# Optimization experiments

Hardware: AMD Instinct MI355X
Metric: run time of the kernel (lower is better)

The kernel has to match this reference:

```python
import jax, jax.numpy as jnp
import numpy as np

B, T = 4, 8192
C = 64            # dilation_channels (also embedding size)
S = 256           # skip_dims
V = 256           # waveform_categories (8-bit mu-law)
CENTER = 128      # waveform_center_cat
DILATIONS = [1, 2, 4, 8, 16, 32, 64, 128, 256, 512] * 3  # 3 blocks, 30 layers
L = len(DILATIONS)


def setup_inputs() -> dict:
    key = jax.random.key(0)
    ks = jax.random.split(key, 16)
    waveform = jax.random.randint(ks[0], (B, T, 1), 0, V, dtype=jnp.int32)
    waveform_lens = jax.random.randint(ks[1], (B,), 0, T, dtype=jnp.int32)
    s = 0.05
    embed = jax.random.normal(ks[2], (V, C), dtype=jnp.float32) * s
    # conv_w[l, 0] applies to x[t-d], conv_w[l, 1] to x[t] (kernel_size=2)
    conv_w = jax.random.normal(ks[3], (L, 2, C, 2 * C), dtype=jnp.float32) * s
    conv_b = jnp.zeros((L, 2 * C), dtype=jnp.float32)
    res_w = jax.random.normal(ks[4], (L, C, C), dtype=jnp.float32) * s
    res_b = jnp.zeros((L, C), dtype=jnp.float32)
    skip_w = jax.random.normal(ks[5], (L, C, S), dtype=jnp.float32) * s
    skip_b = jnp.zeros((L, S), dtype=jnp.float32)
    w0 = jax.random.normal(ks[6], (S, V), dtype=jnp.float32) * s
    b0 = jnp.zeros((V,), dtype=jnp.float32)
    w1 = jax.random.normal(ks[7], (V, V), dtype=jnp.float32) * s
    b1 = jnp.zeros((V,), dtype=jnp.float32)
    return dict(waveform=waveform, waveform_lens=waveform_lens, embed=embed,
                conv_w=conv_w, conv_b=conv_b, res_w=res_w, res_b=res_b,
                skip_w=skip_w, skip_b=skip_b, w0=w0, b0=b0, w1=w1, b1=b1)


def _wavenet(wf, lens, embed, conv_w, conv_b, res_w, res_b, skip_w, skip_b, w0, b0, w1, b1):
    labels = wf[..., 0]                                          # (B, T) int
    # shift right with <go> = center category
    inp = jnp.concatenate(
        [jnp.full((B, 1), CENTER, dtype=labels.dtype), labels[:, :-1]], axis=1)
    x = embed[inp]                                               # (B, T, C)
    skip_sum = jnp.zeros((B, T, S), dtype=x.dtype)
    for i, d in enumerate(DILATIONS):
        # dilated causal conv, kernel 2: y[t] = x[t-d] @ W0 + x[t] @ W1 + b
        x_shift = jnp.pad(x, ((0, 0), (d, 0), (0, 0)))[:, :T]    # left pad d
        h = (jnp.einsum('btc,cf->btf', x_shift, conv_w[i, 0])
             + jnp.einsum('btc,cf->btf', x, conv_w[i, 1]) + conv_b[i])
        gate = jnp.tanh(h[..., :C]) * jax.nn.sigmoid(h[..., C:])  # (B, T, C)
        x = x + jnp.einsum('btc,cd->btd', gate, res_w[i]) + res_b[i]
        skip_sum = skip_sum + jnp.einsum('btc,cs->bts', gate, skip_w[i]) + skip_b[i]
    hid0 = jax.nn.relu(jnp.einsum('bts,sv->btv', skip_sum, w0) + b0)
    logits = jnp.einsum('btv,vu->btu', hid0, w1) + b1            # (B, T, V)
    logp = jax.nn.log_softmax(logits, axis=-1)
    ce = -jnp.take_along_axis(logp, labels[..., None], axis=-1)[..., 0]  # (B, T)
    mask = (jnp.arange(T)[None, :] < lens[:, None]).astype(logits.dtype)
    loss = jnp.sum(ce * mask) / jnp.maximum(jnp.sum(mask), 1.0)
    return loss


def reference(waveform, waveform_lens, embed, conv_w, conv_b, res_w, res_b,
              skip_w, skip_b, w0, b0, w1, b1):
    return _wavenet(waveform, waveform_lens, embed, conv_w, conv_b, res_w,
                    res_b, skip_w, skip_b, w0, b0, w1, b1)
```

## Files before the change

### kernel.cpp

```cpp
#include <hip/hip_runtime.h>

#define NB 4
#define NT 8192
#define NC 64
#define NS 256
#define NV 256
#define NL 30

typedef __attribute__((ext_vector_type(8))) short bf16x8;
typedef __attribute__((ext_vector_type(4))) float f32x4;
typedef unsigned short ushort_t;

#define MFMA(a, b, c) __builtin_amdgcn_mfma_f32_16x16x32_bf16(a, b, c, 0, 0, 0)

#define OFF_WCAT 0
#define SZ_WCAT  (NL * 16384)
#define OFF_RW   (OFF_WCAT + SZ_WCAT)
#define SZ_RW    (NL * 4096)
#define OFF_SWG  (OFF_RW + SZ_RW)
#define SZ_SWG   (6 * 81920)
#define OFF_W0   (OFF_SWG + SZ_SWG)
#define OFF_W1   (OFF_W0 + 65536)
#define TOTAL_W  (OFF_W1 + 65536)
#define N_PREP   (TOTAL_W + 1792)

#define X_ELEMS  (NB * NT * NC)
#define SK_ELEMS (NB * NT * NS)
#define G_ELEMS  (NB * NT * NC)

#define WS_SMALL ((size_t)(2 * X_ELEMS + SK_ELEMS + 5 * G_ELEMS + TOTAL_W) * 2 \
                  + 1792 * 4)
#define WS_BIG   ((size_t)(2 * X_ELEMS + 30 * G_ELEMS + TOTAL_W) * 2 + 1792 * 4)

__device__ inline ushort_t f2bu(float f) {
  union { float f; unsigned u; } v; v.f = f;
  unsigned r = v.u + 0x7FFFu + ((v.u >> 16) & 1u);
  return (ushort_t)(r >> 16);
}
__device__ inline float b2f(ushort_t h) {
  union { unsigned u; float f; } v; v.u = ((unsigned)h) << 16; return v.f;
}

__global__ void sentinel_kernel(float* __restrict__ out) {
  if (threadIdx.x == 0) out[0] = -1234.0f;
}

__global__ __launch_bounds__(256) void prep_kernel(
    const float* __restrict__ cw, const float* __restrict__ rw,
    const float* __restrict__ sw, const float* __restrict__ w0,
    const float* __restrict__ w1, const float* __restrict__ sb_all,
    ushort_t* __restrict__ wt, float* __restrict__ sbg,
    float* __restrict__ out0)
{
  int idx = blockIdx.x * 256 + threadIdx.x;
  if (idx == 0) out0[0] = 0.f;
  if (idx >= N_PREP) return;
  if (idx >= TOTAL_W) {
    int j = idx - TOTAL_W;
    if (j < 1536) {
      int g = j >> 8, n = j & 255;
      float s = 0.f;
#pragma unroll
      for (int jj = 0; jj < 5; ++jj) s += sb_all[(5 * g + jj) * 256 + n];
      sbg[j] = s;
    } else {
      int n = j - 1536;
      float s = 0.f;
      for (int jj = 0; jj < NL; ++jj) s += sb_all[jj * 256 + n];
      sbg[j] = s;
    }
    return;
  }
  float v;
  if (idx < OFF_RW) {
    int e = idx; int l = e >> 14; int r = e & 16383;
    int kk = r >> 12, n = (r >> 5) & 127, j = r & 31;
    int k = kk * 32 + j, tap = k >> 6, c = k & 63;
    v = cw[(((l * 2 + tap) << 6) + c) * 128 + n];
  } else if (idx < OFF_SWG) {
    int e = idx - OFF_RW; int l = e >> 12; int r = e & 4095;
    int kk = r >> 11, n = (r >> 5) & 63, j = r & 31;
    int k = kk * 32 + j;
    v = rw[((l << 6) + k) * 64 + n];
  } else if (idx < OFF_W0) {
    int e = idx - OFF_SWG; int g = e / 81920; int r = e % 81920;
    int kk = r >> 13; int rem = r & 8191;
    int n = rem >> 5, jj = rem & 31;
    int k = kk * 32 + jj;
    v = sw[(size_t)(320 * g + k) * 256 + n];
  } else if (idx < OFF_W1) {
    int e = idx - OFF_W0;
    int kk = e >> 13; int rem = e & 8191;
    int n = rem >> 5, jj = rem & 31;
    int k = kk * 32 + jj;
    v = w0[k * 256 + n];
  } else {
    int e = idx - OFF_W1;
    int kk = e >> 13; int rem = e & 8191;
    int n = rem >> 5, jj = rem & 31;
    int k = kk * 32 + jj;
    v = w1[k * 256 + n];
  }
  wt[idx] = f2bu(v);
}

__global__ __launch_bounds__(256) void embed_kernel(
    const int* __restrict__ wf, const float* __restrict__ embed,
    ushort_t* __restrict__ x0)
{
  const int bidx = blockIdx.x;
  const int bb = bidx >> 7;
  const int t0 = (bidx & 127) << 6;
  const int pos0 = bb * NT + t0;
  for (int e = threadIdx.x; e < 64 * 64; e += 256) {
    int p = e >> 6, c = e & 63;
    int t = t0 + p;
    int id = (t == 0) ? 128 : wf[bb * NT + t - 1];
    x0[(size_t)(pos0 + p) * NC + c] = f2bu(embed[id * NC + c]);
  }
}

__global__ __launch_bounds__(384) void chain5_kernel(
    const ushort_t* __restrict__ xin, ushort_t* __restrict__ xout,
    ushort_t* __restrict__ gates,
    const ushort_t* __restrict__ wt,
    const float* __restrict__ cb_all, const float* __restrict__ rb_all,
    int l0, const int* __restrict__ wf, const float* __restrict__ embf)
{
  __shared__ __align__(16) ushort_t xt[96][72];
  __shared__ __align__(16) ushort_t gt[96][72];

  const int tid = threadIdx.x;
  const int w = tid >> 6, lane = tid & 63;
  const int quad = lane >> 4, c16 = lane & 15;
  const int bb = blockIdx.x >> 7;
  const int t0 = (blockIdx.x & 127) << 6;
  const size_t row0 = (size_t)bb * NT;

#pragma unroll
  for (int i = 0; i < 2; ++i) {
    int e = tid + i * 384;
    int r = e >> 3, c0 = (e & 7) * 8;
    int t = t0 - 32 + r;
    bf16x8 v;
    if (t >= 0) {
      if (embf) {
        int id = (t == 0) ? 128 : wf[row0 + t - 1];
        const float* ep = embf + id * NC + c0;
#pragma unroll
        for (int jj = 0; jj < 8; ++jj) v[jj] = (short)f2bu(ep[jj]);
      } else {
        v = *(const bf16x8*)(xin + (row0 + t) * 64 + c0);
      }
    } else { bf16x8 z = {0, 0, 0, 0, 0, 0, 0, 0}; v = z; }
    *(bf16x8*)&xt[r][c0] = v;
  }
  __syncthreads();

  for (int j = 0; j < 5; ++j) {
    const int l = l0 + j;
    const int d = 1 << j;
    const ushort_t* wcat = wt + OFF_WCAT + l * 16384;
    const ushort_t* rww  = wt + OFF_RW + l * 4096;
    const float* cb = cb_all + l * 128;
    const float* rb = rb_all + l * 64;

    bf16x8 af[4];
    {
      int lr = w * 16 + c16;
#pragma unroll
      for (int kk = 0; kk < 4; ++kk) {
        int rr = (kk < 2) ? lr - d : lr;
        int ch = (kk & 1) * 32 + quad * 8;
        if (rr >= 0) af[kk] = *(const bf16x8*)&xt[rr][ch];
        else { bf16x8 z = {0, 0, 0, 0, 0, 0, 0, 0}; af[kk] = z; }
      }
    }
    __syncthreads();

    {
      f32x4 acc[8];
#pragma unroll
      for (int q = 0; q < 4; ++q) {
        float ba = cb[q * 16 + c16], bs = cb[q * 16 + c16 + 64];
        f32x4 va = {ba, ba, ba, ba}, vb = {bs, bs, bs, bs};
        acc[q] = va; acc[4 + q] = vb;
      }
#pragma unroll
      for (int kk = 0; kk < 4; ++kk) {
        const ushort_t* wp = wcat + kk * 4096 + c16 * 32 + quad * 8;
#pragma unroll
        for (int q = 0; q < 4; ++q) {
          acc[q]     = MFMA(af[kk], *(const bf16x8*)(wp + q * 512), acc[q]);
          acc[4 + q] = MFMA(af[kk], *(const bf16x8*)(wp + q * 512 + 2048), acc[4 + q]);
        }
      }
#pragma unroll
      for (int q = 0; q < 4; ++q)
#pragma unroll
        for (int r = 0; r < 4; ++r) {
          float e2 = __expf(2.f * acc[q][r]);
          float th = (e2 - 1.f) / (e2 + 1.f);
          float sg = 1.f / (1.f + __expf(-acc[4 + q][r]));
          gt[w * 16 + quad * 4 + r][q * 16 + c16] = f2bu(th * sg);
        }

      bf16x8 gf0 = *(const bf16x8*)&gt[w * 16 + c16][quad * 8];
      bf16x8 gf1 = *(const bf16x8*)&gt[w * 16 + c16][32 + quad * 8];

      f32x4 acc2[4];
#pragma unroll
      for (int q = 0; q < 4; ++q) {
        float bv = rb[q * 16 + c16];
        f32x4 z = {bv, bv, bv, bv};
        acc2[q] = z;
      }
      const ushort_t* wp2 = rww + c16 * 32 + quad * 8;
#pragma unroll
      for (int q = 0; q < 4; ++q)
        acc2[q] = MFMA(gf0, *(const bf16x8*)(wp2 + q * 512), acc2[q]);
#pragma unroll
      for (int q = 0; q < 4; ++q)
        acc2[q] = MFMA(gf1, *(const bf16x8*)(wp2 + q * 512 + 2048), acc2[q]);
#pragma unroll
      for (int q = 0; q < 4; ++q) {
        int n = q * 16 + c16;
#pragma unroll
        for (int r = 0; r < 4; ++r) {
          int rowi = w * 16 + quad * 4 + r;
          xt[rowi][n] = f2bu(b2f(xt[rowi][n]) + acc2[q][r]);
        }
      }
    }
    __syncthreads();

    {
      ushort_t* gslot = gates + (size_t)j * G_ELEMS;
      int e = tid;
      {
        int r = e >> 3, c0 = (e & 7) * 8;
        *(bf16x8*)(gslot + (row0 + t0 + r) * 64 + c0) =
            *(const bf16x8*)&gt[32 + r][c0];
      }
      e = tid + 384;
      if (e < 512) {
        int r = e >> 3, c0 = (e & 7) * 8;
        *(bf16x8*)(gslot + (row0 + t0 + r) * 64 + c0) =
            *(const bf16x8*)&gt[32 + r][c0];
      }
    }
  }
  __syncthreads();

  {
    int e = tid;
    {
      int r = e >> 3, c0 = (e & 7) * 8;
      *(bf16x8*)(xout + (row0 + t0 + r) * 64 + c0) = *(const bf16x8*)&xt[32 + r][c0];
    }
    e = tid + 384;
    if (e < 512) {
      int r = e >> 3, c0 = (e & 7) * 8;
      *(bf16x8*)(xout + (row0 + t0 + r) * 64 + c0) = *(const bf16x8*)&xt[32 + r][c0];
    }
  }
}

__global__ __launch_bounds__(256, 4) void layer_kernel(
    const ushort_t* __restrict__ xin, ushort_t* __restrict__ xout,
    ushort_t* __restrict__ gate_out,
    const ushort_t* __restrict__ wcat_s, const float* __restrict__ cb,
    const ushort_t* __restrict__ rww,    const float* __restrict__ rb,
    int d, int write_res)
{
  __shared__ __align__(16) ushort_t lwc[16384];
  __shared__ __align__(16) ushort_t gt[64][72];

  const int tid = threadIdx.x;
  const int w = tid >> 6, lane = tid & 63;
  const int quad = lane >> 4, c16 = lane & 15;
  const int bb = blockIdx.x >> 7;
  const int t0 = (blockIdx.x & 127) << 6;
  const int tb = t0 + w * 16;
  const size_t row0 = (size_t)bb * NT;

  {
    bf16x8* dst = (bf16x8*)lwc;
    const bf16x8* s1 = (const bf16x8*)wcat_s;
#pragma unroll
    for (int i = 0; i < 8; ++i) dst[tid + i * 256] = s1[tid + i * 256];
  }

  const int tA = tb + c16;
  bf16x8 af[4];
#pragma unroll
  for (int kk = 0; kk < 4; ++kk) {
    int ts = (kk < 2) ? (tA - d) : tA;
    int ch = (kk & 1) * 32 + quad * 8;
    if (ts >= 0) {
      af[kk] = *(const bf16x8*)(xin + (row0 + ts) * 64 + ch);
    } else {
      bf16x8 z = {0, 0, 0, 0, 0, 0, 0, 0};
      af[kk] = z;
    }
  }
  __syncthreads();

#pragma unroll
  for (int q = 0; q < 4; ++q) {
    int na = q * 16 + c16;
    int nb2 = na + 64;
    float ba = cb[na], bs = cb[nb2];
    f32x4 va = {ba, ba, ba, ba}, vb = {bs, bs, bs, bs};
#pragma unroll
    for (int kk = 0; kk < 4; ++kk) {
      va = MFMA(af[kk], *(const bf16x8*)&lwc[kk * 4096 + na * 32 + quad * 8], va);
      vb = MFMA(af[kk], *(const bf16x8*)&lwc[kk * 4096 + nb2 * 32 + quad * 8], vb);
    }
#pragma unroll
    for (int r = 0; r < 4; ++r) {
      float e2 = __expf(2.f * va[r]);
      float th = (e2 - 1.f) / (e2 + 1.f);
      float sg = 1.f / (1.f + __expf(-vb[r]));
      gt[w * 16 + quad * 4 + r][q * 16 + c16] = f2bu(th * sg);
    }
  }

  bf16x8 gf0 = *(const bf16x8*)&gt[w * 16 + c16][quad * 8];
  bf16x8 gf1 = *(const bf16x8*)&gt[w * 16 + c16][32 + quad * 8];

  if (write_res) {
    const ushort_t* wp2 = rww + c16 * 32 + quad * 8;
#pragma unroll
    for (int q = 0; q < 4; ++q) {
      int n = q * 16 + c16;
      float bv = rb[n];
      f32x4 acc = {bv, bv, bv, bv};
      acc = MFMA(gf0, *(const bf16x8*)(wp2 + q * 512), acc);
      acc = MFMA(gf1, *(const bf16x8*)(wp2 + q * 512 + 2048), acc);
#pragma unroll
      for (int r = 0; r < 4; ++r) {
        size_t idx = (row0 + tb + quad * 4 + r) * 64 + n;
        xout[idx] = f2bu(b2f(xin[idx]) + acc[r]);
      }
    }
  }

#pragma unroll
  for (int i = 0; i < 2; ++i) {
    int e = lane + i * 64;
    int rr = w * 16 + (e >> 3), c0 = (e & 7) * 8;
    *(bf16x8*)(gate_out + (row0 + t0 + rr) * 64 + c0) = *(const bf16x8*)&gt[rr][c0];
  }
}

__global__ __launch_bounds__(384) void chain5hi_kernel(
    const ushort_t* __restrict__ xin, ushort_t* __restrict__ xout,
    ushort_t* __restrict__ gates,
    const ushort_t* __restrict__ wt,
    const float* __restrict__ cb_all, const float* __restrict__ rb_all,
    int lbase, int write_x)
{
  __shared__ __align__(16) ushort_t xt[96][72];
  __shared__ __align__(16) ushort_t gt[96][72];

  const int tid = threadIdx.x;
  const int w = tid >> 6, lane = tid & 63;
  const int quad = lane >> 4, c16 = lane & 15;
  const int bb = blockIdx.x >> 7;
  const int sub = blockIdx.x & 127;
  const int k = sub & 31;
  const int i0 = (sub >> 5) << 6;
  const size_t row0 = (size_t)bb * NT;

#pragma unroll
  for (int i = 0; i < 2; ++i) {
    int e = tid + i * 384;
    int r = e >> 3, c0 = (e & 7) * 8;
    int ii = i0 + r - 32;
    bf16x8 v;
    if (ii >= 0) v = *(const bf16x8*)(xin + (row0 + (size_t)ii * 32 + k) * 64 + c0);
    else { bf16x8 z = {0, 0, 0, 0, 0, 0, 0, 0}; v = z; }
    *(bf16x8*)&xt[r][c0] = v;
  }
  __syncthreads();

  for (int j = 0; j < 5; ++j) {
    const int l = lbase + j;
    const int d = 1 << j;
    const ushort_t* wcat = wt + OFF_WCAT + l * 16384;
    const ushort_t* rww  = wt + OFF_RW + l * 4096;
    const float* cb = cb_all + l * 128;
    const float* rb = rb_all + l * 64;

    bf16x8 af[4];
    {
      int lr = w * 16 + c16;
#pragma unroll
      for (int kk = 0; kk < 4; ++kk) {
        int rr = (kk < 2) ? lr - d : lr;
        int ch = (kk & 1) * 32 + quad * 8;
        if (rr >= 0) af[kk] = *(const bf16x8*)&xt[rr][ch];
        else { bf16x8 z = {0, 0, 0, 0, 0, 0, 0, 0}; af[kk] = z; }
      }
    }
    __syncthreads();

    {
      f32x4 acc[8];
#pragma unroll
      for (int q = 0; q < 4; ++q) {
        float ba = cb[q * 16 + c16], bs = cb[q * 16 + c16 + 64];
        f32x4 va = {ba, ba, ba, ba}, vb = {bs, bs, bs, bs};
        acc[q] = va; acc[4 + q] = vb;
      }
#pragma unroll
      for (int kk = 0; kk < 4; ++kk) {
        const ushort_t* wp = wcat + kk * 4096 + c16 * 32 + quad * 8;
#pragma unroll
        for (int q = 0; q < 4; ++q) {
          acc[q]     = MFMA(af[kk], *(const bf16x8*)(wp + q * 512), acc[q]);
          acc[4 + q] = MFMA(af[kk], *(const bf16x8*)(wp + q * 512 + 2048), acc[4 + q]);
        }
      }
#pragma unroll
      for (int q = 0; q < 4; ++q)
#pragma unroll
        for (int r = 0; r < 4; ++r) {
          float e2 = __expf(2.f * acc[q][r]);
          float th = (e2 - 1.f) / (e2 + 1.f);
          float sg = 1.f / (1.f + __expf(-acc[4 + q][r]));
          gt[w * 16 + quad * 4 + r][q * 16 + c16] = f2bu(th * sg);
        }

      if (write_x || j < 4) {
        bf16x8 gf0 = *(const bf16x8*)&gt[w * 16 + c16][quad * 8];
        bf16x8 gf1 = *(const bf16x8*)&gt[w * 16 + c16][32 + quad * 8];

        f32x4 acc2[4];
#pragma unroll
        for (int q = 0; q < 4; ++q) {
          float bv = rb[q * 16 + c16];
          f32x4 z = {bv, bv, bv, bv};
          acc2[q] = z;
        }
        const ushort_t* wp2 = rww + c16 * 32 + quad * 8;
#pragma unroll
        for (int q = 0; q < 4; ++q)
          acc2[q] = MFMA(gf0, *(const bf16x8*)(wp2 + q * 512), acc2[q]);
#pragma unroll
        for (int q = 0; q < 4; ++q)
          acc2[q] = MFMA(gf1, *(const bf16x8*)(wp2 + q * 512 + 2048), acc2[q]);
#pragma unroll
        for (int q = 0; q < 4; ++q) {
          int n = q * 16 + c16;
#pragma unroll
          for (int r = 0; r < 4; ++r) {
            int rowi = w * 16 + quad * 4 + r;
            xt[rowi][n] = f2bu(b2f(xt[rowi][n]) + acc2[q][r]);
          }
        }
      }
    }
    __syncthreads();

    {
      ushort_t* gslot = gates + (size_t)j * G_ELEMS;
      int e = tid;
      {
        int r = e >> 3, c0 = (e & 7) * 8;
        *(bf16x8*)(gslot + (row0 + (size_t)(i0 + r) * 32 + k) * 64 + c0) =
            *(const bf16x8*)&gt[32 + r][c0];
      }
      e = tid + 384;
      if (e < 512) {
        int r = e >> 3, c0 = (e & 7) * 8;
        *(bf16x8*)(gslot + (row0 + (size_t)(i0 + r) * 32 + k) * 64 + c0) =
            *(const bf16x8*)&gt[32 + r][c0];
      }
    }
  }
  __syncthreads();

  if (write_x) {
    int e = tid;
    {
      int r = e >> 3, c0 = (e & 7) * 8;
      *(bf16x8*)(xout + (row0 + (size_t)(i0 + r) * 32 + k) * 64 + c0) =
          *(const bf16x8*)&xt[32 + r][c0];
    }
    e = tid + 384;
    if (e < 512) {
      int r = e >> 3, c0 = (e & 7) * 8;
      *(bf16x8*)(xout + (row0 + (size_t)(i0 + r) * 32 + k) * 64 + c0) =
          *(const bf16x8*)&xt[32 + r][c0];
    }
  }
}

__global__ __launch_bounds__(256) void skip30_head_kernel(
    const ushort_t* __restrict__ gates,
    const ushort_t* __restrict__ wt,
    const float* __restrict__ sbtot,
    const float* __restrict__ b0, const float* __restrict__ b1,
    const int* __restrict__ wf, const int* __restrict__ lens,
    float* __restrict__ loss)
{
  __shared__ __align__(16) ushort_t wbuf[2][8192];
  __shared__ __align__(16) ushort_t tile[64][264];
  const int tid = threadIdx.x;
  const int w = tid >> 6, lane = tid & 63;
  const int quad = lane >> 4, c16 = lane & 15;
  const int bb = blockIdx.x >> 7;
  const int t0 = (blockIdx.x & 127) << 6;
  const int tb = t0 + w * 16;
  const size_t row0 = (size_t)bb * NT;
  const int mylen = lens[bb];
  const ushort_t* swg = wt + OFF_SWG;

  f32x4 acc[16];
#pragma unroll
  for (int nt = 0; nt < 16; ++nt) { f32x4 z = {0.f, 0.f, 0.f, 0.f}; acc[nt] = z; }

  const size_t arow = (row0 + tb + c16) * 64;
  bf16x8 wreg[4];
#pragma unroll
  for (int i = 0; i < 4; ++i)
    wreg[i] = ((const bf16x8*)swg)[tid + i * 256];
  bf16x8 af = *(const bf16x8*)(gates + arow + quad * 8);
  int cur = 0;

  for (int kk = 0; kk < 60; ++kk) {
#pragma unroll
    for (int i = 0; i < 4; ++i)
      ((bf16x8*)wbuf[cur])[tid + i * 256] = wreg[i];
    int kn = (kk + 1 < 60) ? kk + 1 : 59;
#pragma unroll
    for (int i = 0; i < 4; ++i)
      wreg[i] = ((const bf16x8*)(swg + (size_t)kn * 8192))[tid + i * 256];
    bf16x8 afn = *(const bf16x8*)(gates + (size_t)(kn >> 1) * G_ELEMS + arow +
                                  (kn & 1) * 32 + quad * 8);
    __syncthreads();
    const ushort_t* wp = wbuf[cur] + c16 * 32 + quad * 8;
#pragma unroll
    for (int nt = 0; nt < 16; ++nt)
      acc[nt] = MFMA(af, *(const bf16x8*)(wp + nt * 512), acc[nt]);
    af = afn; cur ^= 1;
  }

#pragma unroll
  for (int nt = 0; nt < 16; ++nt) {
    int n = nt * 16 + c16;
    float sbn = sbtot[n];
#pragma unroll
    for (int r = 0; r < 4; ++r)
      tile[w * 16 + quad * 4 + r][n] = f2bu(acc[nt][r] + sbn);
  }

  const ushort_t* w0T = wt + OFF_W0;
  f32x4 accA[16];
#pragma unroll
  for (int nt = 0; nt < 16; ++nt) {
    float bv = b0[nt * 16 + c16];
    f32x4 z = {bv, bv, bv, bv};
    accA[nt] = z;
  }
  for (int kk = 0; kk < 8; ++kk) {
#pragma unroll
    for (int i = 0; i < 4; ++i)
      ((bf16x8*)wbuf[0])[tid + i * 256] = ((const bf16x8*)(w0T + kk * 8192))[tid + i * 256];
    __syncthreads();
    bf16x8 hf = *(const bf16x8*)&tile[w * 16 + c16][kk * 32 + quad * 8];
    const ushort_t* wp = wbuf[0] + c16 * 32 + quad * 8;
#pragma unroll
    for (int nt = 0; nt < 16; ++nt)
      accA[nt] = MFMA(hf, *(const bf16x8*)(wp + nt * 512), accA[nt]);
    __syncthreads();
  }
#pragma unroll
  for (int nt = 0; nt < 16; ++nt)
#pragma unroll
    for (int r = 0; r < 4; ++r)
      tile[w * 16 + quad * 4 + r][nt * 16 + c16] = f2bu(fmaxf(accA[nt][r], 0.f));

  const ushort_t* w1T = wt + OFF_W1;
  f32x4 acc2[16];
#pragma unroll
  for (int nt = 0; nt < 16; ++nt) {
    float bv = b1[nt * 16 + c16];
    f32x4 z = {bv, bv, bv, bv};
    acc2[nt] = z;
  }
  for (int kk = 0; kk < 8; ++kk) {
#pragma unroll
    for (int i = 0; i < 4; ++i)
      ((bf16x8*)wbuf[0])[tid + i * 256] = ((const bf16x8*)(w1T + kk * 8192))[tid + i * 256];
    __syncthreads();
    bf16x8 hf = *(const bf16x8*)&tile[w * 16 + c16][kk * 32 + quad * 8];
    const ushort_t* wp = wbuf[0] + c16 * 32 + quad * 8;
#pragma unroll
    for (int nt = 0; nt < 16; ++nt)
      acc2[nt] = MFMA(hf, *(const bf16x8*)(wp + nt * 512), acc2[nt]);
    __syncthreads();
  }

  int lblv[4];
#pragma unroll
  for (int r = 0; r < 4; ++r)
    lblv[r] = wf[row0 + tb + quad * 4 + r];

  float local = 0.f;
#pragma unroll
  for (int r = 0; r < 4; ++r) {
    float m = -1e30f, tv = -1e30f;
#pragma unroll
    for (int nt = 0; nt < 16; ++nt) {
      float v = acc2[nt][r];
      m = fmaxf(m, v);
      if (lblv[r] == nt * 16 + c16) tv = v;
    }
#pragma unroll
    for (int dd = 1; dd < 16; dd <<= 1) m = fmaxf(m, __shfl_xor(m, dd));
    float s = 0.f;
#pragma unroll
    for (int nt = 0; nt < 16; ++nt) s += __expf(acc2[nt][r] - m);
#pragma unroll
    for (int dd = 1; dd < 16; dd <<= 1) {
      s += __shfl_xor(s, dd);
      tv = fmaxf(tv, __shfl_xor(tv, dd));
    }
    int t = tb + quad * 4 + r;
    if (c16 == 0 && t < mylen) local += (m + __logf(s)) - tv;
  }
#pragma unroll
  for (int dd = 1; dd < 64; dd <<= 1) local += __shfl_xor(local, dd);
  if (lane == 0 && local != 0.f) atomicAdd(loss, local);
}

__global__ __launch_bounds__(256) void skip_kernel(
    ushort_t* __restrict__ skip, const ushort_t* __restrict__ gates,
    const ushort_t* __restrict__ swg, const float* __restrict__ sbg,
    int first)
{
  __shared__ __align__(16) ushort_t wbuf[8192];
  const int tid = threadIdx.x;
  const int w = tid >> 6, lane = tid & 63;
  const int quad = lane >> 4, c16 = lane & 15;
  const int bb = blockIdx.x >> 7;
  const int t0 = (blockIdx.x & 127) << 6;
  const int tb = t0 + w * 16;
  const size_t row0 = (size_t)bb * NT;

  f32x4 acc[16];
#pragma unroll
  for (int nt = 0; nt < 16; ++nt) { f32x4 z = {0.f, 0.f, 0.f, 0.f}; acc[nt] = z; }

  const size_t arow = (row0 + tb + c16) * 64;
  for (int kk = 0; kk < 10; ++kk) {
#pragma unroll
    for (int i = 0; i < 4; ++i)
      ((bf16x8*)wbuf)[tid + i * 256] = ((const bf16x8*)(swg + kk * 8192))[tid + i * 256];
    __syncthreads();

    int slot = kk >> 1;
    bf16x8 af = *(const bf16x8*)(gates + (size_t)slot * G_ELEMS + arow +
                                 (kk & 1) * 32 + quad * 8);
    const ushort_t* wp = wbuf + c16 * 32 + quad * 8;
#pragma unroll
    for (int nt = 0; nt < 16; ++nt)
      acc[nt] = MFMA(af, *(const bf16x8*)(wp + nt * 512), acc[nt]);
    __syncthreads();
  }

#pragma unroll
  for (int nt = 0; nt < 16; ++nt) {
    int n = nt * 16 + c16;
    float sbn = sbg[n];
#pragma unroll
    for (int r = 0; r < 4; ++r) {
      size_t idx = (row0 + tb + quad * 4 + r) * 256 + n;
      float old = first ? 0.f : b2f(skip[idx]);
      skip[idx] = f2bu(old + acc[nt][r] + sbn);
    }
  }
}

__global__ __launch_bounds__(256) void head_kernel(
    const ushort_t* __restrict__ skip,
    const ushort_t* __restrict__ w0T, const float* __restrict__ b0,
    const ushort_t* __restrict__ w1T, const float* __restrict__ b1,
    const int* __restrict__ wf, const int* __restrict__ lens,
    float* __restrict__ loss)
{
  __shared__ __align__(16) ushort_t wbuf[8192];
  __shared__ __align__(16) ushort_t tile[64][264];
  const int tid = threadIdx.x;
  const int w = tid >> 6, lane = tid & 63;
  const int quad = lane >> 4, c16 = lane & 15;
  const int bb = blockIdx.x >> 7;
  const int t0 = (blockIdx.x & 127) << 6;
  const int tb = t0 + w * 16;
  const size_t row0 = (size_t)bb * NT;
  const int mylen = lens[bb];

#pragma unroll
  for (int i = 0; i < 8; ++i) {
    int e = lane + i * 64;
    int r = e >> 5, c0 = (e & 31) * 8;
    *(bf16x8*)&tile[w * 16 + r][c0] =
        *(const bf16x8*)(skip + (row0 + t0 + w * 16 + r) * 256 + c0);
  }

  f32x4 accA[16];
#pragma unroll
  for (int nt = 0; nt < 16; ++nt) {
    float bv = b0[nt * 16 + c16];
    f32x4 z = {bv, bv, bv, bv};
    accA[nt] = z;
  }
  for (int kk = 0; kk < 8; ++kk) {
#pragma unroll
    for (int i = 0; i < 4; ++i)
      ((bf16x8*)wbuf)[tid + i * 256] = ((const bf16x8*)(w0T + kk * 8192))[tid + i * 256];
    __syncthreads();
    bf16x8 af = *(const bf16x8*)&tile[w * 16 + c16][kk * 32 + quad * 8];
    const ushort_t* wp = wbuf + c16 * 32 + quad * 8;
#pragma unroll
    for (int nt = 0; nt < 16; ++nt)
      accA[nt] = MFMA(af, *(const bf16x8*)(wp + nt * 512), accA[nt]);
    __syncthreads();
  }
#pragma unroll
  for (int nt = 0; nt < 16; ++nt)
#pragma unroll
    for (int r = 0; r < 4; ++r)
      tile[w * 16 + quad * 4 + r][nt * 16 + c16] = f2bu(fmaxf(accA[nt][r], 0.f));

  f32x4 acc2[16];
#pragma unroll
  for (int nt = 0; nt < 16; ++nt) {
    float bv = b1[nt * 16 + c16];
    f32x4 z = {bv, bv, bv, bv};
    acc2[nt] = z;
  }
  for (int kk = 0; kk < 8; ++kk) {
#pragma unroll
    for (int i = 0; i < 4; ++i)
      ((bf16x8*)wbuf)[tid + i * 256] = ((const bf16x8*)(w1T + kk * 8192))[tid + i * 256];
    __syncthreads();
    bf16x8 hf = *(const bf16x8*)&tile[w * 16 + c16][kk * 32 + quad * 8];
    const ushort_t* wp = wbuf + c16 * 32 + quad * 8;
#pragma unroll
    for (int nt = 0; nt < 16; ++nt)
      acc2[nt] = MFMA(hf, *(const bf16x8*)(wp + nt * 512), acc2[nt]);
    __syncthreads();
  }

  int lblv[4];
#pragma unroll
  for (int r = 0; r < 4; ++r)
    lblv[r] = wf[row0 + tb + quad * 4 + r];

  float local = 0.f;
#pragma unroll
  for (int r = 0; r < 4; ++r) {
    float m = -1e30f, tv = -1e30f;
#pragma unroll
    for (int nt = 0; nt < 16; ++nt) {
      float v = acc2[nt][r];
      m = fmaxf(m, v);
      if (lblv[r] == nt * 16 + c16) tv = v;
    }
#pragma unroll
    for (int dd = 1; dd < 16; dd <<= 1) m = fmaxf(m, __shfl_xor(m, dd));
    float s = 0.f;
#pragma unroll
    for (int nt = 0; nt < 16; ++nt) s += __expf(acc2[nt][r] - m);
#pragma unroll
    for (int dd = 1; dd < 16; dd <<= 1) {
      s += __shfl_xor(s, dd);
      tv = fmaxf(tv, __shfl_xor(tv, dd));
    }
    int t = tb + quad * 4 + r;
    if (c16 == 0 && t < mylen) local += (m + __logf(s)) - tv;
  }
#pragma unroll
  for (int dd = 1; dd < 64; dd <<= 1) local += __shfl_xor(local, dd);
  if (lane == 0 && local != 0.f) atomicAdd(loss, local);
}

__global__ void finalize_kernel(const int* __restrict__ lens,
                                float* __restrict__ out)
{
  if (threadIdx.x == 0) {
    float den = 0.f;
    for (int b = 0; b < NB; ++b) {
      int l = lens[b];
      if (l > NT) l = NT;
      den += (float)l;
    }
    out[0] = out[0] / fmaxf(den, 1.f);
  }
}

extern "C" void kernel_launch(void* const* d_in, const int* in_sizes, int n_in,
                              void* d_out, int out_size, void* d_ws, size_t ws_size,
                              hipStream_t stream) {
  const int*   wf     = (const int*)d_in[0];
  const int*   lens   = (const int*)d_in[1];
  const float* embed  = (const float*)d_in[2];
  const float* conv_w = (const float*)d_in[3];
  const float* conv_b = (const float*)d_in[4];
  const float* res_w  = (const float*)d_in[5];
  const float* res_b  = (const float*)d_in[6];
  const float* skip_w = (const float*)d_in[7];
  const float* skip_b = (const float*)d_in[8];
  const float* w0     = (const float*)d_in[9];
  const float* b0     = (const float*)d_in[10];
  const float* w1     = (const float*)d_in[11];
  const float* b1     = (const float*)d_in[12];

  float* out = (float*)d_out;
  if (ws_size < WS_SMALL) {
    sentinel_kernel<<<1, 64, 0, stream>>>(out);
    return;
  }
  const bool big = (ws_size >= WS_BIG);

  static const int dil[NL] = {1, 2, 4, 8, 16, 32, 64, 128, 256, 512,
                              1, 2, 4, 8, 16, 32, 64, 128, 256, 512,
                              1, 2, 4, 8, 16, 32, 64, 128, 256, 512};

  if (big) {
    ushort_t* x0    = (ushort_t*)d_ws;
    ushort_t* x1    = x0 + X_ELEMS;
    ushort_t* gates = x1 + X_ELEMS;
    ushort_t* wt    = gates + 30 * (size_t)G_ELEMS;
    float*    sbg   = (float*)(wt + TOTAL_W);

    prep_kernel<<<(N_PREP + 255) / 256, 256, 0, stream>>>(
        conv_w, res_w, skip_w, w0, w1, skip_b, wt, sbg, out);

    const ushort_t* xin = x0;
    ushort_t* xout = x1;
    for (int blk = 0; blk < 3; ++blk) {
      const int l0 = blk * 10;
      chain5_kernel<<<512, 384, 0, stream>>>(
          xin, xout, gates + (size_t)l0 * G_ELEMS,
          wt, conv_b, res_b, l0, wf, blk == 0 ? embed : nullptr);
      { const ushort_t* t = xout; xout = (ushort_t*)xin; xin = t; }
      for (int l = l0 + 5; l < l0 + 10; ++l) {
        layer_kernel<<<512, 256, 0, stream>>>(
            xin, xout, gates + (size_t)l * G_ELEMS,
            wt + OFF_WCAT + l * 16384, conv_b + l * 128,
            wt + OFF_RW + l * 4096,    res_b + l * 64,
            dil[l], l < NL - 1 ? 1 : 0);
        { const ushort_t* t = xout; xout = (ushort_t*)xin; xin = t; }
      }
    }

    skip30_head_kernel<<<512, 256, 0, stream>>>(
        gates, wt, sbg + 1536, b0, b1, wf, lens, out);
    finalize_kernel<<<1, 64, 0, stream>>>(lens, out);
  } else {
    ushort_t* x0    = (ushort_t*)d_ws;
    ushort_t* x1    = x0 + X_ELEMS;
    ushort_t* skip  = x1 + X_ELEMS;
    ushort_t* gates = skip + SK_ELEMS;
    ushort_t* wt    = gates + 5 * (size_t)G_ELEMS;
    float*    sbg   = (float*)(wt + TOTAL_W);

    prep_kernel<<<(N_PREP + 255) / 256, 256, 0, stream>>>(
        conv_w, res_w, skip_w, w0, w1, skip_b, wt, sbg, out);
    embed_kernel<<<512, 256, 0, stream>>>(wf, embed, x0);

    const ushort_t* xin = x0;
    ushort_t* xout = x1;
    for (int blk = 0; blk < 3; ++blk) {
      const int l0 = blk * 10;
      chain5_kernel<<<512, 384, 0, stream>>>(
          xin, xout, gates, wt, conv_b, res_b, l0, wf, nullptr);
      { const ushort_t* t = xout; xout = (ushort_t*)xin; xin = t; }
      skip_kernel<<<512, 256, 0, stream>>>(
          skip, gates, wt + OFF_SWG + (size_t)(2 * blk) * 81920,
          sbg + (size_t)(2 * blk) * 256, blk == 0 ? 1 : 0);
      chain5hi_kernel<<<512, 384, 0, stream>>>(
          xin, xout, gates, wt, conv_b, res_b, l0 + 5, blk < 2 ? 1 : 0);
      { const ushort_t* t = xout; xout = (ushort_t*)xin; xin = t; }
      skip_kernel<<<512, 256, 0, stream>>>(
          skip, gates, wt + OFF_SWG + (size_t)(2 * blk + 1) * 81920,
          sbg + (size_t)(2 * blk + 1) * 256, 0);
    }

    head_kernel<<<512, 256, 0, stream>>>(
        skip, wt + OFF_W0, b0, wt + OFF_W1, b1, wf, lens, out);
    finalize_kernel<<<1, 64, 0, stream>>>(lens, out);
  }
}
```

Measured before the change: 416.3 us.

## Fuse high-dilation layers into strided chain kernels keeping residual in LDS

Replaces the five per-layer launches for dilations 32..512 with two fused kernels (2 and 3 layers) that gather a strided time subsequence (stride 32 or 128) so each dilation becomes a small local shift within an LDS tile. The residual stream stays in shared memory across the fused layers and is written out once, which cuts launches and global round trips of x. It adds halo recomputation (80 rows loaded for 64 outputs), strided global access patterns, and reads weights directly from global instead of staging them in LDS.

Result: slower. 435.2 us (+4.5%).

```diff
diff --git a/kernel.cpp b/kernel.cpp
--- a/kernel.cpp
+++ b/kernel.cpp
@@ -266,91 +266,273 @@
   }
 }
 
-__global__ __launch_bounds__(256, 4) void layer_kernel(
+__global__ __launch_bounds__(320) void chain2hi_kernel(
     const ushort_t* __restrict__ xin, ushort_t* __restrict__ xout,
-    ushort_t* __restrict__ gate_out,
-    const ushort_t* __restrict__ wcat_s, const float* __restrict__ cb,
-    const ushort_t* __restrict__ rww,    const float* __restrict__ rb,
-    int d, int write_res)
+    ushort_t* __restrict__ gates,
+    const ushort_t* __restrict__ wt,
+    const float* __restrict__ cb_all, const float* __restrict__ rb_all,
+    int lbase)
 {
-  __shared__ __align__(16) ushort_t lwc[16384];
-  __shared__ __align__(16) ushort_t gt[64][72];
+  __shared__ __align__(16) ushort_t xt[80][72];
+  __shared__ __align__(16) ushort_t gt[80][72];
 
   const int tid = threadIdx.x;
   const int w = tid >> 6, lane = tid & 63;
   const int quad = lane >> 4, c16 = lane & 15;
   const int bb = blockIdx.x >> 7;
-  const int t0 = (blockIdx.x & 127) << 6;
-  const int tb = t0 + w * 16;
+  const int sub = blockIdx.x & 127;
+  const int k = sub & 31;
+  const int i0 = (sub >> 5) << 6;
   const size_t row0 = (size_t)bb * NT;
 
-  {
-    bf16x8* dst = (bf16x8*)lwc;
-    const bf16x8* s1 = (const bf16x8*)wcat_s;
-#pragma unroll
-    for (int i = 0; i < 8; ++i) dst[tid + i * 256] = s1[tid + i * 256];
-  }
-
-  const int tA = tb + c16;
-  bf16x8 af[4];
-#pragma unroll
-  for (int kk = 0; kk < 4; ++kk) {
-    int ts = (kk < 2) ? (tA - d) : tA;
-    int ch = (kk & 1) * 32 + quad * 8;
-    if (ts >= 0) {
-      af[kk] = *(const bf16x8*)(xin + (row0 + ts) * 64 + ch);
-    } else {
-      bf16x8 z = {0, 0, 0, 0, 0, 0, 0, 0};
-      af[kk] = z;
-    }
+#pragma unroll
+  for (int i = 0; i < 2; ++i) {
+    int e = tid + i * 320;
+    int r = e >> 3, c0 = (e & 7) * 8;
+    int ii = i0 + r - 16;
+    bf16x8 v;
+    if (ii >= 0) v = *(const bf16x8*)(xin + (row0 + (size_t)ii * 32 + k) * 64 + c0);
+    else { bf16x8 z = {0, 0, 0, 0, 0, 0, 0, 0}; v = z; }
+    *(bf16x8*)&xt[r][c0] = v;
   }
   __syncthreads();
 
-#pragma unroll
-  for (int q = 0; q < 4; ++q) {
-    int na = q * 16 + c16;
-    int nb2 = na + 64;
-    float ba = cb[na], bs = cb[nb2];
-    f32x4 va = {ba, ba, ba, ba}, vb = {bs, bs, bs, bs};
-#pragma unroll
-    for (int kk = 0; kk < 4; ++kk) {
-      va = MFMA(af[kk], *(const bf16x8*)&lwc[kk * 4096 + na * 32 + quad * 8], va);
-      vb = MFMA(af[kk], *(const bf16x8*)&lwc[kk * 4096 + nb2 * 32 + quad * 8], vb);
-    }
-#pragma unroll
-    for (int r = 0; r < 4; ++r) {
-      float e2 = __expf(2.f * va[r]);
-      float th = (e2 - 1.f) / (e2 + 1.f);
-      float sg = 1.f / (1.f + __expf(-vb[r]));
-      gt[w * 16 + quad * 4 + r][q * 16 + c16] = f2bu(th * sg);
-    }
-  }
-
-  bf16x8 gf0 = *(const bf16x8*)&gt[w * 16 + c16][quad * 8];
-  bf16x8 gf1 = *(const bf16x8*)&gt[w * 16 + c16][32 + quad * 8];
-
-  if (write_res) {
-    const ushort_t* wp2 = rww + c16 * 32 + quad * 8;
-#pragma unroll
-    for (int q = 0; q < 4; ++q) {
-      int n = q * 16 + c16;
-      float bv = rb[n];
-      f32x4 acc = {bv, bv, bv, bv};
-      acc = MFMA(gf0, *(const bf16x8*)(wp2 + q * 512), acc);
-      acc = MFMA(gf1, *(const bf16x8*)(wp2 + q * 512 + 2048), acc);
-#pragma unroll
-      for (int r = 0; r < 4; ++r) {
-        size_t idx = (row0 + tb + quad * 4 + r) * 64 + n;
-        xout[idx] = f2bu(b2f(xin[idx]) + acc[r]);
-      }
-    }
-  }
+  for (int j = 0; j < 2; ++j) {
+    const int l = lbase + j;
+    const int d = 1 << j;
+    const ushort_t* wcat = wt + OFF_WCAT + l * 16384;
+    const ushort_t* rww  = wt + OFF_RW + l * 4096;
+    const float* cb = cb_all + l * 128;
+    const float* rb = rb_all + l * 64;
+
+    bf16x8 af[4];
+    {
+      int lr = w * 16 + c16;
+#pragma unroll
+      for (int kk = 0; kk < 4; ++kk) {
+        int rr = (kk < 2) ? lr - d : lr;
+        int ch = (kk & 1) * 32 + quad * 8;
+        if (rr >= 0) af[kk] = *(const bf16x8*)&xt[rr][ch];
+        else { bf16x8 z = {0, 0, 0, 0, 0, 0, 0, 0}; af[kk] = z; }
+      }
+    }
+    __syncthreads();
+
+    {
+      f32x4 acc[8];
+#pragma unroll
+      for (int q = 0; q < 4; ++q) {
+        float ba = cb[q * 16 + c16], bs = cb[q * 16 + c16 + 64];
+        f32x4 va = {ba, ba, ba, ba}, vb = {bs, bs, bs, bs};
+        acc[q] = va; acc[4 + q] = vb;
+      }
+#pragma unroll
+      for (int kk = 0; kk < 4; ++kk) {
+        const ushort_t* wp = wcat + kk * 4096 + c16 * 32 + quad * 8;
+#pragma unroll
+        for (int q = 0; q < 4; ++q) {
+          acc[q]     = MFMA(af[kk], *(const bf16x8*)(wp + q * 512), acc[q]);
+          acc[4 + q] = MFMA(af[kk], *(const bf16x8*)(wp + q * 512 + 2048), acc[4 + q]);
+        }
+      }
+#pragma unroll
+      for (int q = 0; q < 4; ++q)
+#pragma unroll
+        for (int r = 0; r < 4; ++r) {
+          float e2 = __expf(2.f * acc[q][r]);
+          float th = (e2 - 1.f) / (e2 + 1.f);
+          float sg = 1.f / (1.f + __expf(-acc[4 + q][r]));
+          gt[w * 16 + quad * 4 + r][q * 16 + c16] = f2bu(th * sg);
+        }
+
+      bf16x8 gf0 = *(const bf16x8*)&gt[w * 16 + c16][quad * 8];
+      bf16x8 gf1 = *(const bf16x8*)&gt[w * 16 + c16][32 + quad * 8];
+
+      f32x4 acc2[4];
+#pragma unroll
+      for (int q = 0; q < 4; ++q) {
+        float bv = rb[q * 16 + c16];
+        f32x4 z = {bv, bv, bv, bv};
+        acc2[q] = z;
+      }
+      const ushort_t* wp2 = rww + c16 * 32 + quad * 8;
+#pragma unroll
+      for (int q = 0; q < 4; ++q)
+        acc2[q] = MFMA(gf0, *(const bf16x8*)(wp2 + q * 512), acc2[q]);
+#pragma unroll
+      for (int q = 0; q < 4; ++q)
+        acc2[q] = MFMA(gf1, *(const bf16x8*)(wp2 + q * 512 + 2048), acc2[q]);
+#pragma unroll
+      for (int q = 0; q < 4; ++q) {
+        int n = q * 16 + c16;
+#pragma unroll
+        for (int r = 0; r < 4; ++r) {
+          int rowi = w * 16 + quad * 4 + r;
+          xt[rowi][n] = f2bu(b2f(xt[rowi][n]) + acc2[q][r]);
+        }
+      }
+    }
+    __syncthreads();
+
+    {
+      ushort_t* gslot = gates + (size_t)l * G_ELEMS;
+#pragma unroll
+      for (int i = 0; i < 2; ++i) {
+        int e = tid + i * 320;
+        if (e < 512) {
+          int r = e >> 3, c0 = (e & 7) * 8;
+          *(bf16x8*)(gslot + (row0 + (size_t)(i0 + r) * 32 + k) * 64 + c0) =
+              *(const bf16x8*)&gt[16 + r][c0];
+        }
+      }
+    }
+  }
+  __syncthreads();
 
 #pragma unroll
   for (int i = 0; i < 2; ++i) {
-    int e = lane + i * 64;
-    int rr = w * 16 + (e >> 3), c0 = (e & 7) * 8;
-    *(bf16x8*)(gate_out + (row0 + t0 + rr) * 64 + c0) = *(const bf16x8*)&gt[rr][c0];
+    int e = tid + i * 320;
+    if (e < 512) {
+      int r = e >> 3, c0 = (e & 7) * 8;
+      *(bf16x8*)(xout + (row0 + (size_t)(i0 + r) * 32 + k) * 64 + c0) =
+          *(const bf16x8*)&xt[16 + r][c0];
+    }
+  }
+}
+
+__global__ __launch_bounds__(320) void chain3hi_kernel(
+    const ushort_t* __restrict__ xin, ushort_t* __restrict__ xout,
+    ushort_t* __restrict__ gates,
+    const ushort_t* __restrict__ wt,
+    const float* __restrict__ cb_all, const float* __restrict__ rb_all,
+    int lbase, int write_x)
+{
+  __shared__ __align__(16) ushort_t xt[80][72];
+  __shared__ __align__(16) ushort_t gt[80][72];
+
+  const int tid = threadIdx.x;
+  const int w = tid >> 6, lane = tid & 63;
+  const int quad = lane >> 4, c16 = lane & 15;
+  const int bb = blockIdx.x >> 7;
+  const int k2 = blockIdx.x & 127;
+  const size_t row0 = (size_t)bb * NT;
+
+#pragma unroll
+  for (int i = 0; i < 2; ++i) {
+    int e = tid + i * 320;
+    int r = e >> 3, c0 = (e & 7) * 8;
+    int ii = r - 16;
+    bf16x8 v;
+    if (ii >= 0) v = *(const bf16x8*)(xin + (row0 + (size_t)ii * 128 + k2) * 64 + c0);
+    else { bf16x8 z = {0, 0, 0, 0, 0, 0, 0, 0}; v = z; }
+    *(bf16x8*)&xt[r][c0] = v;
+  }
+  __syncthreads();
+
+  for (int j = 0; j < 3; ++j) {
+    const int l = lbase + j;
+    const int d = 1 << j;
+    const ushort_t* wcat = wt + OFF_WCAT + l * 16384;
+    const ushort_t* rww  = wt + OFF_RW + l * 4096;
+    const float* cb = cb_all + l * 128;
+    const float* rb = rb_all + l * 64;
+
+    bf16x8 af[4];
+    {
+      int lr = w * 16 + c16;
+#pragma unroll
+      for (int kk = 0; kk < 4; ++kk) {
+        int rr = (kk < 2) ? lr - d : lr;
+        int ch = (kk & 1) * 32 + quad * 8;
+        if (rr >= 0) af[kk] = *(const bf16x8*)&xt[rr][ch];
+        else { bf16x8 z = {0, 0, 0, 0, 0, 0, 0, 0}; af[kk] = z; }
+      }
+    }
+    __syncthreads();
+
+    {
+      f32x4 acc[8];
+#pragma unroll
+      for (int q = 0; q < 4; ++q) {
+        float ba = cb[q * 16 + c16], bs = cb[q * 16 + c16 + 64];
+        f32x4 va = {ba, ba, ba, ba}, vb = {bs, bs, bs, bs};
+        acc[q] = va; acc[4 + q] = vb;
+      }
+#pragma unroll
+      for (int kk = 0; kk < 4; ++kk) {
+        const ushort_t* wp = wcat + kk * 4096 + c16 * 32 + quad * 8;
+#pragma unroll
+        for (int q = 0; q < 4; ++q) {
+          acc[q]     = MFMA(af[kk], *(const bf16x8*)(wp + q * 512), acc[q]);
+          acc[4 + q] = MFMA(af[kk], *(const bf16x8*)(wp + q * 512 + 2048), acc[4 + q]);
+        }
+      }
+#pragma unroll
+      for (int q = 0; q < 4; ++q)
+#pragma unroll
+        for (int r = 0; r < 4; ++r) {
+          float e2 = __expf(2.f * acc[q][r]);
+          float th = (e2 - 1.f) / (e2 + 1.f);
+          float sg = 1.f / (1.f + __expf(-acc[4 + q][r]));
+          gt[w * 16 + quad * 4 + r][q * 16 + c16] = f2bu(th * sg);
+        }
+
+      if (write_x || j < 2) {
+        bf16x8 gf0 = *(const bf16x8*)&gt[w * 16 + c16][quad * 8];
+        bf16x8 gf1 = *(const bf16x8*)&gt[w * 16 + c16][32 + quad * 8];
+
+        f32x4 acc2[4];
+#pragma unroll
+        for (int q = 0; q < 4; ++q) {
+          float bv = rb[q * 16 + c16];
+          f32x4 z = {bv, bv, bv, bv};
+          acc2[q] = z;
+        }
+        const ushort_t* wp2 = rww + c16 * 32 + quad * 8;
+#pragma unroll
+        for (int q = 0; q < 4; ++q)
+          acc2[q] = MFMA(gf0, *(const bf16x8*)(wp2 + q * 512), acc2[q]);
+#pragma unroll
+        for (int q = 0; q < 4; ++q)
+          acc2[q] = MFMA(gf1, *(const bf16x8*)(wp2 + q * 512 + 2048), acc2[q]);
+#pragma unroll
+        for (int q = 0; q < 4; ++q) {
+          int n = q * 16 + c16;
+#pragma unroll
+          for (int r = 0; r < 4; ++r) {
+            int rowi = w * 16 + quad * 4 + r;
+            xt[rowi][n] = f2bu(b2f(xt[rowi][n]) + acc2[q][r]);
+          }
+        }
+      }
+    }
+    __syncthreads();
+
+    {
+      ushort_t* gslot = gates + (size_t)l * G_ELEMS;
+#pragma unroll
+      for (int i = 0; i < 2; ++i) {
+        int e = tid + i * 320;
+        if (e < 512) {
+          int r = e >> 3, c0 = (e & 7) * 8;
+          *(bf16x8*)(gslot + (row0 + (size_t)r * 128 + k2) * 64 + c0) =
+              *(const bf16x8*)&gt[16 + r][c0];
+        }
+      }
+    }
+  }
+  __syncthreads();
+
+  if (write_x) {
+#pragma unroll
+    for (int i = 0; i < 2; ++i) {
+      int e = tid + i * 320;
+      if (e < 512) {
+        int r = e >> 3, c0 = (e & 7) * 8;
+        *(bf16x8*)(xout + (row0 + (size_t)r * 128 + k2) * 64 + c0) =
+            *(const bf16x8*)&xt[16 + r][c0];
+      }
+    }
   }
 }
 
@@ -827,10 +1009,6 @@
   }
   const bool big = (ws_size >= WS_BIG);
 
-  static const int dil[NL] = {1, 2, 4, 8, 16, 32, 64, 128, 256, 512,
-                              1, 2, 4, 8, 16, 32, 64, 128, 256, 512,
-                              1, 2, 4, 8, 16, 32, 64, 128, 256, 512};
-
   if (big) {
     ushort_t* x0    = (ushort_t*)d_ws;
     ushort_t* x1    = x0 + X_ELEMS;
@@ -849,14 +1027,12 @@
           xin, xout, gates + (size_t)l0 * G_ELEMS,
           wt, conv_b, res_b, l0, wf, blk == 0 ? embed : nullptr);
       { const ushort_t* t = xout; xout = (ushort_t*)xin; xin = t; }
-      for (int l = l0 + 5; l < l0 + 10; ++l) {
-        layer_kernel<<<512, 256, 0, stream>>>(
-            xin, xout, gates + (size_t)l * G_ELEMS,
-            wt + OFF_WCAT + l * 16384, conv_b + l * 128,
-            wt + OFF_RW + l * 4096,    res_b + l * 64,
-            dil[l], l < NL - 1 ? 1 : 0);
-        { const ushort_t* t = xout; xout = (ushort_t*)xin; xin = t; }
-      }
+      chain2hi_kernel<<<512, 320, 0, stream>>>(
+          xin, xout, gates, wt, conv_b, res_b, l0 + 5);
+      { const ushort_t* t = xout; xout = (ushort_t*)xin; xin = t; }
+      chain3hi_kernel<<<512, 320, 0, stream>>>(
+          xin, xout, gates, wt, conv_b, res_b, l0 + 7, blk < 2 ? 1 : 0);
+      { const ushort_t* t = xout; xout = (ushort_t*)xin; xin = t; }
     }
 
     skip30_head_kernel<<<512, 256, 0, stream>>>(
```
